# Performance work log

Measured on AMD Instinct MI355X. Metric: run time of the kernel, lower is better.

Reference implementation:

```python
import jax, jax.numpy as jnp
import numpy as np

NUM_HEADS = 16
HEAD_SIZE = 64
MAX_POS = 2048  # config.max_position_embeddings


def setup_inputs() -> dict:
    key = jax.random.key(0)
    ks = jax.random.split(key, 8)
    B, Lq, Lk, D = 4, 1024, 2048, 1024
    s = 1.0 / np.sqrt(D)
    return {
        "hidden_states": jax.random.normal(ks[0], (B, Lk, D), jnp.float32),
        "query_hidden_states": jax.random.normal(ks[1], (B, Lq, D), jnp.float32),
        "attention_mask": jnp.zeros((B, 1, 1, Lk), jnp.float32),
        "Wq": jax.random.normal(ks[2], (D, D), jnp.float32) * s,
        "bq": jnp.zeros((D,), jnp.float32),
        "Wk": jax.random.normal(ks[3], (D, D), jnp.float32) * s,
        "bk": jnp.zeros((D,), jnp.float32),
        "Wv": jax.random.normal(ks[4], (D, D), jnp.float32) * s,
        "bv": jnp.zeros((D,), jnp.float32),
        "dist_emb": jax.random.normal(ks[5], (2 * MAX_POS - 1, HEAD_SIZE), jnp.float32) * 0.02,
    }


def _split_heads(x):
    # [B, L, H*Dh] -> [B, H, L, Dh]
    B, L, _ = x.shape
    return x.reshape(B, L, NUM_HEADS, HEAD_SIZE).transpose(0, 2, 1, 3)


def reference(hidden_states, query_hidden_states, attention_mask, Wq, bq, Wk, bk, Wv, bv, dist_emb):
    # Linear projections (torch Linear: x @ W.T + b)
    q = _split_heads(query_hidden_states @ Wq.T + bq)   # [B,H,Lq,Dh]
    k = _split_heads(hidden_states @ Wk.T + bk)          # [B,H,Lk,Dh]
    v = _split_heads(hidden_states @ Wv.T + bv)          # [B,H,Lk,Dh]

    scores = jnp.einsum('bhld,bhrd->bhlr', q, k)         # [B,H,Lq,Lk]

    # relative_key_query positional scores
    Lq, Lk = q.shape[2], k.shape[2]
    distance = jnp.arange(Lq)[:, None] - jnp.arange(Lk)[None, :]
    pe = dist_emb[distance + MAX_POS - 1]                # [Lq,Lk,Dh]
    scores = scores + jnp.einsum('bhld,lrd->bhlr', q, pe) + jnp.einsum('bhrd,lrd->bhlr', k, pe)

    scores = scores / np.sqrt(HEAD_SIZE) + attention_mask
    probs = jax.nn.softmax(scores, axis=-1)              # dropout p=0 (eval)
    ctx = jnp.einsum('bhlr,bhrd->bhld', probs, v)        # [B,H,Lq,Dh]
    B = ctx.shape[0]
    return ctx.transpose(0, 2, 1, 3).reshape(B, Lq, NUM_HEADS * HEAD_SIZE)
```

## Files before the change

### kernel.cpp

```cpp
#include <hip/hip_runtime.h>
#include <hip/hip_bf16.h>

#define B_   4
#define H_   16
#define LQ   1024
#define LK   2048
#define D_   1024
#define DH   64

typedef __attribute__((ext_vector_type(8))) short  short8;
typedef __attribute__((ext_vector_type(4))) float  float4_;
typedef __attribute__((ext_vector_type(4))) unsigned int uint4_;

static __device__ __forceinline__ float bf2f(unsigned short u) {
    unsigned int x = ((unsigned int)u) << 16;
    return __builtin_bit_cast(float, x);
}
static __device__ __forceinline__ unsigned short f2bf(float f) {
    unsigned int x = __builtin_bit_cast(unsigned int, f);
    unsigned int lsb = (x >> 16) & 1u;
    x += 0x7fffu + lsb;
    return (unsigned short)(x >> 16);
}
static __device__ __forceinline__ unsigned int pack2(float a, float b) {
    __hip_bfloat162 h = __float22bfloat162_rn(make_float2(a, b));
    unsigned int r;
    __builtin_memcpy(&r, &h, 4);
    return r;
}

#define MFMA(a, b, c) __builtin_amdgcn_mfma_f32_16x16x32_bf16((a), (b), (c), 0, 0, 0)

#define G2ROW(tl) ((tl) * 144 + ((tl) >> 2) * 8)

__global__ __launch_bounds__(256) void conv_kernel(
    const float* __restrict__ Wq, const float* __restrict__ Wk,
    const float* __restrict__ Wv, const float* __restrict__ Eg,
    unsigned short* __restrict__ cWq, unsigned short* __restrict__ cWk,
    unsigned short* __restrict__ cWv, unsigned short* __restrict__ cEb)
{
    int bid = blockIdx.x;
    const float* src; unsigned short* dst; int nch;
    if (bid < 512)       { src = Wq; dst = cWq;              nch = 131072; }
    else if (bid < 1024) { src = Wk; dst = cWk; bid -= 512;  nch = 131072; }
    else if (bid < 1536) { src = Wv; dst = cWv; bid -= 1024; nch = 131072; }
    else                 { src = Eg; dst = cEb; bid -= 1536; nch = 32760;  }
    int ch = bid * 256 + threadIdx.x;
    if (ch >= nch) return;
    const float* s = src + (size_t)ch * 8;
    float4_ v0 = *(const float4_*)s, v1 = *(const float4_*)(s + 4);
    uint4_ o;
    o[0] = pack2(v0[0], v0[1]); o[1] = pack2(v0[2], v0[3]);
    o[2] = pack2(v1[0], v1[1]); o[3] = pack2(v1[2], v1[3]);
    *(uint4_*)(dst + (size_t)ch * 8) = o;
}

__global__ __launch_bounds__(256) void proj_kernel(
    const float* __restrict__ Xq, const float* __restrict__ Xk,
    const unsigned short* __restrict__ Wq, const float* __restrict__ bq,
    const unsigned short* __restrict__ Wk, const float* __restrict__ bk,
    const unsigned short* __restrict__ Wv, const float* __restrict__ bv,
    unsigned short* __restrict__ Qh, unsigned short* __restrict__ Kh,
    unsigned short* __restrict__ VT)
{
    __shared__ short smem[17408];
    short* As = smem;
    short* Bs = smem + 5120;
    short* Cs = smem;

    int bid = blockIdx.x;
    int which, tm, tn;
    const float *X, *bias; const unsigned short* W;
    if (bid < 256)      { which = 0; int t = bid;       tm = t >> 3; tn = t & 7; X = Xq; W = Wq; bias = bq; }
    else if (bid < 768) { which = 1; int t = bid - 256; tm = t >> 3; tn = t & 7; X = Xk; W = Wk; bias = bk; }
    else                { which = 2; int t = bid - 768; tm = t >> 3; tn = t & 7; X = Xk; W = Wv; bias = bv; }

    int tid  = threadIdx.x;
    int wave = tid >> 6, lane = tid & 63;
    int wr = (wave >> 1) * 64, wc = (wave & 1) * 64;
    int m0 = tm * 128, n0 = tn * 128;

    float4_ acc[4][4];
    for (int a = 0; a < 4; ++a) for (int c = 0; c < 4; ++c) acc[a][c] = (float4_)0.0f;

    int srow = tid >> 2, skp = (tid & 3) * 8;
    const float*          Ag = X + (size_t)(m0 + srow) * D_ + skp;
    const unsigned short* Bg = W + (size_t)(n0 + srow) * D_ + skp;
    int lrow = lane & 15, lk8 = (lane >> 4) * 8;

    for (int kt = 0; kt < 32; ++kt) {
        int k0 = kt * 32;
        for (int i = 0; i < 2; ++i) {
            int row = srow + i * 64;
            const float* pa = Ag + (size_t)i * 64 * D_ + k0;
            float4_ a0 = *(const float4_*)(pa);
            float4_ a1 = *(const float4_*)(pa + 4);
            uint4_ va;
            va[0] = pack2(a0[0], a0[1]); va[1] = pack2(a0[2], a0[3]);
            va[2] = pack2(a1[0], a1[1]); va[3] = pack2(a1[2], a1[3]);
            uint4_ vb = *(const uint4_*)(Bg + (size_t)i * 64 * D_ + k0);
            *(uint4_*)(&As[row * 40 + skp]) = va;
            *(uint4_*)(&Bs[row * 40 + skp]) = vb;
        }
        __syncthreads();
        short8 af[4], bfr[4];
        for (int rt = 0; rt < 4; ++rt) af[rt]  = *(const short8*)(&As[(wr + rt * 16 + lrow) * 40 + lk8]);
        for (int ct = 0; ct < 4; ++ct) bfr[ct] = *(const short8*)(&Bs[(wc + ct * 16 + lrow) * 40 + lk8]);
        for (int rt = 0; rt < 4; ++rt)
            for (int ct = 0; ct < 4; ++ct)
                acc[rt][ct] = MFMA(af[rt], bfr[ct], acc[rt][ct]);
        __syncthreads();
    }

    int lrow4 = (lane >> 4) * 4, lcol = lane & 15;
    if (which < 2) {
        int lsh = (which == 0) ? 10 : 11;
        int Lm1 = (1 << lsh) - 1;
        unsigned short* dst = (which == 0) ? Qh : Kh;
        for (int rt = 0; rt < 4; ++rt)
            for (int ct = 0; ct < 4; ++ct)
                for (int i = 0; i < 4; ++i) {
                    int m = m0 + wr + rt * 16 + lrow4 + i;
                    int n = n0 + wc + ct * 16 + lcol;
                    float v = acc[rt][ct][i] + bias[n];
                    int b = m >> lsh, s = m & Lm1;
                    int h = n >> 6, d = n & 63;
                    dst[((size_t)((b * H_ + h) << lsh) + (size_t)s) * DH + d] = f2bf(v);
                }
    } else {
        for (int rt = 0; rt < 4; ++rt)
            for (int ct = 0; ct < 4; ++ct)
                for (int i = 0; i < 4; ++i) {
                    int rl = wr + rt * 16 + lrow4 + i;
                    int cl = wc + ct * 16 + lcol;
                    float v = acc[rt][ct][i] + bias[n0 + cl];
                    Cs[cl * 136 + rl] = (short)f2bf(v);
                }
        __syncthreads();
        int b = m0 >> 11, r0 = m0 & 2047;
        int c = tid >> 1, half = tid & 1;
        int n = n0 + c, h = n >> 6, d = n & 63;
        unsigned short* dstp = VT + ((size_t)(b * H_ + h) * DH + d) * LK + r0 + half * 64;
        for (int j = 0; j < 8; ++j) {
            uint4_ v = *(const uint4_*)(&Cs[c * 136 + half * 64 + j * 8]);
            *(uint4_*)(dstp + j * 8) = v;
        }
    }
}

__global__ __launch_bounds__(256, 2) void attn_kernel(
    const unsigned short* __restrict__ Qh, const unsigned short* __restrict__ Kh,
    const unsigned short* __restrict__ VT, const unsigned short* __restrict__ Eb,
    const float* __restrict__ mask, float* __restrict__ out)
{
    __shared__ short smem[27776];
    short* Qs  = smem;
    short* Ks  = smem;
    short* VTs = smem + 4608;
    short* Es  = smem + 9216;
    short* G2  = smem + 18432;
    short* Ps  = G2;

    int bid = blockIdx.x;
    int l0 = (bid & 15) * 64;
    int bh = bid >> 4;
    int b  = bh >> 4, h = bh & 15;
    int tid = threadIdx.x, wave = tid >> 6, lane = tid & 63;
    int lr = lane & 15, lk8 = (lane >> 4) * 8, lr4 = (lane >> 4) * 4;

    for (int i = 0; i < 2; ++i) {
        int idx = tid + 256 * i, row = idx >> 3, g = (idx & 7) * 8;
        *(uint4_*)(&Qs[row * 72 + g]) =
            *(const uint4_*)(Qh + ((size_t)(bh * LQ + l0 + row)) * DH + g);
    }
    __syncthreads();
    short8 aq0 = *(const short8*)(&Qs[(wave * 16 + lr) * 72 + lk8]);
    short8 aq1 = *(const short8*)(&Qs[(wave * 16 + lr) * 72 + 32 + lk8]);

    float m_i[4], l_i[4];
    float4_ Oacc[4];
    for (int i = 0; i < 4; ++i) { m_i[i] = -1e30f; l_i[i] = 0.f; Oacc[i] = (float4_)0.f; }

    const unsigned short* Kbase = Kh + (size_t)bh * LK * DH;
    const unsigned short* Vbase = VT + (size_t)bh * DH * LK;

    int srow = tid >> 3;
    int sg   = (tid & 7) * 8;

    uint4_ kr0, kr1, vr0, vr1, er0, er1, er2, er3;
    auto load_tiles = [&](int it2) {
        int r0_ = it2 * 64, jb_ = l0 - r0_ + 1984;
        kr0 = *(const uint4_*)(Kbase + (size_t)(r0_ + srow) * DH + sg);
        kr1 = *(const uint4_*)(Kbase + (size_t)(r0_ + srow + 32) * DH + sg);
        vr0 = *(const uint4_*)(Vbase + (size_t)srow * LK + r0_ + sg);
        vr1 = *(const uint4_*)(Vbase + (size_t)(srow + 32) * LK + r0_ + sg);
        er0 = *(const uint4_*)(Eb + (size_t)(jb_ + srow) * DH + sg);
        er1 = *(const uint4_*)(Eb + (size_t)(jb_ + srow + 32) * DH + sg);
        er2 = *(const uint4_*)(Eb + (size_t)(jb_ + srow + 64) * DH + sg);
        er3 = *(const uint4_*)(Eb + (size_t)(jb_ + srow + 96) * DH + sg);
    };
    load_tiles(0);

    for (int it = 0; it < 32; ++it) {
        int r0 = it * 64;

        __syncthreads();
        *(uint4_*)(&Ks[srow * 72 + sg])         = kr0;
        *(uint4_*)(&Ks[(srow + 32) * 72 + sg])  = kr1;
        *(uint4_*)(&VTs[srow * 72 + sg])        = vr0;
        *(uint4_*)(&VTs[(srow + 32) * 72 + sg]) = vr1;
        *(uint4_*)(&Es[srow * 72 + sg])         = er0;
        *(uint4_*)(&Es[(srow + 32) * 72 + sg])  = er1;
        *(uint4_*)(&Es[(srow + 64) * 72 + sg])  = er2;
        *(uint4_*)(&Es[(srow + 96) * 72 + sg])  = er3;
        __syncthreads();
        if (it < 31) load_tiles(it + 1);

        float4_ Sacc[4];
        for (int c = 0; c < 4; ++c) {
            short8 b0 = *(const short8*)(&Ks[(c * 16 + lr) * 72 + lk8]);
            short8 b1 = *(const short8*)(&Ks[(c * 16 + lr) * 72 + 32 + lk8]);
            float4_ s = (float4_)0.f;
            s = MFMA(aq0, b0, s);
            s = MFMA(aq1, b1, s);
            Sacc[c] = s;
        }

        short8 ak0 = *(const short8*)(&Ks[(wave * 16 + lr) * 72 + lk8]);
        short8 ak1 = *(const short8*)(&Ks[(wave * 16 + lr) * 72 + 32 + lk8]);
        unsigned int gqp[5][2], gkp[5][2];
        for (int tt = 0; tt < 5; ++tt) {
            int tqi = wave + tt;
            short8 e0 = *(const short8*)(&Es[(tqi * 16 + lr) * 72 + lk8]);
            short8 e1 = *(const short8*)(&Es[(tqi * 16 + lr) * 72 + 32 + lk8]);
            float4_ g = (float4_)0.f;
            g = MFMA(aq0, e0, g); g = MFMA(aq1, e1, g);
            gqp[tt][0] = pack2(g[0], g[1]); gqp[tt][1] = pack2(g[2], g[3]);
            int tk = (3 - wave) + tt;
            short8 f0 = *(const short8*)(&Es[(tk * 16 + lr) * 72 + lk8]);
            short8 f1 = *(const short8*)(&Es[(tk * 16 + lr) * 72 + 32 + lk8]);
            float4_ gg = (float4_)0.f;
            gg = MFMA(ak0, f0, gg); gg = MFMA(ak1, f1, gg);
            gkp[tt][0] = pack2(gg[0], gg[1]); gkp[tt][1] = pack2(gg[2], gg[3]);
        }

        for (int tt = 0; tt < 5; ++tt) {
            int uq = (wave + tt) * 16 + lr;
            int uk = (3 - wave + tt) * 16 + lr;
            for (int i = 0; i < 4; ++i) {
                int row = wave * 16 + lr4 + i;
                unsigned int wq32 = gqp[tt][i >> 1], wk32 = gkp[tt][i >> 1];
                unsigned short vq = (unsigned short)((i & 1) ? (wq32 >> 16) : (wq32 & 0xffff));
                unsigned short vk = (unsigned short)((i & 1) ? (wk32 >> 16) : (wk32 & 0xffff));
                int tr = row - uq + 63;
                if ((unsigned)tr < 64u)
                    G2[G2ROW(row) + ((tr & 15) << 3) + (((tr >> 4)) << 1)] = (short)vq;
                int tl = uk + row - 63;
                if ((unsigned)tl < 64u)
                    G2[G2ROW(tl) + ((row & 15) << 3) + (((row >> 4)) << 1) + 1] = (short)vk;
            }
        }
        __syncthreads();

        float mk[4];
        for (int c = 0; c < 4; ++c) mk[c] = mask[b * LK + r0 + c * 16 + lr];
        for (int i = 0; i < 4; ++i) {
            int tl = wave * 16 + lr4 + i;
            short8 gv = *(const short8*)(&G2[G2ROW(tl) + (lr << 3)]);
            float scv[4], mx = -1e30f;
            for (int c = 0; c < 4; ++c) {
                float sq = bf2f((unsigned short)gv[2 * c]);
                float sk = bf2f((unsigned short)gv[2 * c + 1]);
                float sc = (Sacc[c][i] + sq + sk) * 0.125f + mk[c];
                scv[c] = sc;
                mx = fmaxf(mx, sc);
            }
            for (int off = 1; off < 16; off <<= 1) mx = fmaxf(mx, __shfl_xor(mx, off, 64));
            float mnew = fmaxf(m_i[i], mx);
            float alpha = __expf(m_i[i] - mnew);
            m_i[i] = mnew;
            float e0 = __expf(scv[0] - mnew), e1 = __expf(scv[1] - mnew);
            float e2 = __expf(scv[2] - mnew), e3 = __expf(scv[3] - mnew);
            unsigned int p01 = pack2(e0, e1), p23 = pack2(e2, e3);
            float rs = bf2f((unsigned short)(p01 & 0xffff)) + bf2f((unsigned short)(p01 >> 16))
                     + bf2f((unsigned short)(p23 & 0xffff)) + bf2f((unsigned short)(p23 >> 16));
            for (int off = 1; off < 16; off <<= 1) rs += __shfl_xor(rs, off, 64);
            l_i[i] = l_i[i] * alpha + rs;
            for (int nt = 0; nt < 4; ++nt) Oacc[nt][i] *= alpha;
            Ps[G2ROW(tl) +  0 + lr] = (short)(unsigned short)(p01 & 0xffff);
            Ps[G2ROW(tl) + 16 + lr] = (short)(unsigned short)(p01 >> 16);
            Ps[G2ROW(tl) + 32 + lr] = (short)(unsigned short)(p23 & 0xffff);
            Ps[G2ROW(tl) + 48 + lr] = (short)(unsigned short)(p23 >> 16);
        }
        short8 ap0 = *(const short8*)(&Ps[G2ROW(wave * 16 + lr) + lk8]);
        short8 ap1 = *(const short8*)(&Ps[G2ROW(wave * 16 + lr) + 32 + lk8]);
        for (int nt = 0; nt < 4; ++nt) {
            short8 v0 = *(const short8*)(&VTs[(nt * 16 + lr) * 72 + lk8]);
            short8 v1 = *(const short8*)(&VTs[(nt * 16 + lr) * 72 + 32 + lk8]);
            Oacc[nt] = MFMA(ap0, v0, Oacc[nt]);
            Oacc[nt] = MFMA(ap1, v1, Oacc[nt]);
        }
    }

    for (int nt = 0; nt < 4; ++nt)
        for (int i = 0; i < 4; ++i) {
            int row = l0 + wave * 16 + lr4 + i;
            int col = h * 64 + nt * 16 + lr;
            out[(size_t)(b * LQ + row) * D_ + col] = Oacc[nt][i] / l_i[i];
        }
}

extern "C" void kernel_launch(void* const* d_in, const int* in_sizes, int n_in,
                              void* d_out, int out_size, void* d_ws, size_t ws_size,
                              hipStream_t stream) {
    (void)in_sizes; (void)n_in; (void)out_size; (void)ws_size;
    const float* Xk   = (const float*)d_in[0];
    const float* Xq   = (const float*)d_in[1];
    const float* mask = (const float*)d_in[2];
    const float* Wq   = (const float*)d_in[3];
    const float* bq   = (const float*)d_in[4];
    const float* Wk   = (const float*)d_in[5];
    const float* bk   = (const float*)d_in[6];
    const float* Wv   = (const float*)d_in[7];
    const float* bv   = (const float*)d_in[8];
    const float* Eg   = (const float*)d_in[9];

    unsigned short* Qh  = (unsigned short*)d_ws;
    unsigned short* Kh  = Qh  + (size_t)4194304;
    unsigned short* VT  = Kh  + (size_t)8388608;
    unsigned short* cWq = VT  + (size_t)8388608;
    unsigned short* cWk = cWq + (size_t)1048576;
    unsigned short* cWv = cWk + (size_t)1048576;
    unsigned short* cEb = cWv + (size_t)1048576;
    float* o = (float*)d_out;

    conv_kernel<<<1664, 256, 0, stream>>>(Wq, Wk, Wv, Eg, cWq, cWk, cWv, cEb);
    proj_kernel<<<1280, 256, 0, stream>>>(Xq, Xk, cWq, bq, cWk, bk, cWv, bv, Qh, Kh, VT);
    attn_kernel<<<1024, 256, 0, stream>>>(Qh, Kh, VT, cEb, mask, o);
}
```

Measured before the change: 487.3 us.

## Prefetch projection GEMM tiles and reuse the relative-embedding window as a ring buffer

The projection GEMM now loads the next k-tile into registers while the current tile's MFMAs run, using one barrier per iteration instead of two. The attention kernel keeps the 128-row distance-embedding window in shared memory as a ring buffer indexed by a phase offset. Since the window slides by 64 rows per step, only the 64 new rows are fetched each iteration instead of all 128. The q/k positional MFMAs are merged into one loop that reads each embedding fragment once and feeds both products. This cuts global traffic and LDS reads, at the cost of more live registers and more complex indexing.

```diff
diff --git a/kernel.cpp b/kernel.cpp
--- a/kernel.cpp
+++ b/kernel.cpp
@@ -88,29 +88,40 @@
     const unsigned short* Bg = W + (size_t)(n0 + srow) * D_ + skp;
     int lrow = lane & 15, lk8 = (lane >> 4) * 8;
 
+    float4_ pa0[2], pa1[2]; uint4_ pb[2];
+    auto load_kt = [&](int kt) {
+        int k0 = kt * 32;
+        #pragma unroll
+        for (int i = 0; i < 2; ++i) {
+            const float* pa = Ag + (size_t)i * 64 * D_ + k0;
+            pa0[i] = *(const float4_*)(pa);
+            pa1[i] = *(const float4_*)(pa + 4);
+            pb[i]  = *(const uint4_*)(Bg + (size_t)i * 64 * D_ + k0);
+        }
+    };
+    load_kt(0);
+
     for (int kt = 0; kt < 32; ++kt) {
-        int k0 = kt * 32;
+        __syncthreads();
+        #pragma unroll
         for (int i = 0; i < 2; ++i) {
             int row = srow + i * 64;
-            const float* pa = Ag + (size_t)i * 64 * D_ + k0;
-            float4_ a0 = *(const float4_*)(pa);
-            float4_ a1 = *(const float4_*)(pa + 4);
             uint4_ va;
-            va[0] = pack2(a0[0], a0[1]); va[1] = pack2(a0[2], a0[3]);
-            va[2] = pack2(a1[0], a1[1]); va[3] = pack2(a1[2], a1[3]);
-            uint4_ vb = *(const uint4_*)(Bg + (size_t)i * 64 * D_ + k0);
+            va[0] = pack2(pa0[i][0], pa0[i][1]); va[1] = pack2(pa0[i][2], pa0[i][3]);
+            va[2] = pack2(pa1[i][0], pa1[i][1]); va[3] = pack2(pa1[i][2], pa1[i][3]);
             *(uint4_*)(&As[row * 40 + skp]) = va;
-            *(uint4_*)(&Bs[row * 40 + skp]) = vb;
-        }
-        __syncthreads();
+            *(uint4_*)(&Bs[row * 40 + skp]) = pb[i];
+        }
+        __syncthreads();
+        if (kt < 31) load_kt(kt + 1);
         short8 af[4], bfr[4];
         for (int rt = 0; rt < 4; ++rt) af[rt]  = *(const short8*)(&As[(wr + rt * 16 + lrow) * 40 + lk8]);
         for (int ct = 0; ct < 4; ++ct) bfr[ct] = *(const short8*)(&Bs[(wc + ct * 16 + lrow) * 40 + lk8]);
         for (int rt = 0; rt < 4; ++rt)
             for (int ct = 0; ct < 4; ++ct)
                 acc[rt][ct] = MFMA(af[rt], bfr[ct], acc[rt][ct]);
-        __syncthreads();
-    }
+    }
+    __syncthreads();
 
     int lrow4 = (lane >> 4) * 4, lcol = lane & 15;
     if (which < 2) {
@@ -196,27 +207,35 @@
         vr1 = *(const uint4_*)(Vbase + (size_t)(srow + 32) * LK + r0_ + sg);
         er0 = *(const uint4_*)(Eb + (size_t)(jb_ + srow) * DH + sg);
         er1 = *(const uint4_*)(Eb + (size_t)(jb_ + srow + 32) * DH + sg);
-        er2 = *(const uint4_*)(Eb + (size_t)(jb_ + srow + 64) * DH + sg);
-        er3 = *(const uint4_*)(Eb + (size_t)(jb_ + srow + 96) * DH + sg);
     };
     load_tiles(0);
+    {
+        int jb0 = l0 + 1984;
+        er2 = *(const uint4_*)(Eb + (size_t)(jb0 + srow + 64) * DH + sg);
+        er3 = *(const uint4_*)(Eb + (size_t)(jb0 + srow + 96) * DH + sg);
+    }
 
     for (int it = 0; it < 32; ++it) {
         int r0 = it * 64;
+        int ph = (l0 + 1984 - r0) & 127;
 
         __syncthreads();
         *(uint4_*)(&Ks[srow * 72 + sg])         = kr0;
         *(uint4_*)(&Ks[(srow + 32) * 72 + sg])  = kr1;
         *(uint4_*)(&VTs[srow * 72 + sg])        = vr0;
         *(uint4_*)(&VTs[(srow + 32) * 72 + sg]) = vr1;
-        *(uint4_*)(&Es[srow * 72 + sg])         = er0;
-        *(uint4_*)(&Es[(srow + 32) * 72 + sg])  = er1;
-        *(uint4_*)(&Es[(srow + 64) * 72 + sg])  = er2;
-        *(uint4_*)(&Es[(srow + 96) * 72 + sg])  = er3;
+        *(uint4_*)(&Es[((ph + srow) & 127) * 72 + sg])      = er0;
+        *(uint4_*)(&Es[((ph + srow + 32) & 127) * 72 + sg]) = er1;
+        if (it == 0) {
+            *(uint4_*)(&Es[((ph + srow + 64) & 127) * 72 + sg]) = er2;
+            *(uint4_*)(&Es[((ph + srow + 96) & 127) * 72 + sg]) = er3;
+        }
         __syncthreads();
         if (it < 31) load_tiles(it + 1);
 
+        short8 ak0, ak1;
         float4_ Sacc[4];
+        #pragma unroll
         for (int c = 0; c < 4; ++c) {
             short8 b0 = *(const short8*)(&Ks[(c * 16 + lr) * 72 + lk8]);
             short8 b1 = *(const short8*)(&Ks[(c * 16 + lr) * 72 + 32 + lk8]);
@@ -224,40 +243,47 @@
             s = MFMA(aq0, b0, s);
             s = MFMA(aq1, b1, s);
             Sacc[c] = s;
-        }
-
-        short8 ak0 = *(const short8*)(&Ks[(wave * 16 + lr) * 72 + lk8]);
-        short8 ak1 = *(const short8*)(&Ks[(wave * 16 + lr) * 72 + 32 + lk8]);
-        unsigned int gqp[5][2], gkp[5][2];
-        for (int tt = 0; tt < 5; ++tt) {
-            int tqi = wave + tt;
-            short8 e0 = *(const short8*)(&Es[(tqi * 16 + lr) * 72 + lk8]);
-            short8 e1 = *(const short8*)(&Es[(tqi * 16 + lr) * 72 + 32 + lk8]);
-            float4_ g = (float4_)0.f;
-            g = MFMA(aq0, e0, g); g = MFMA(aq1, e1, g);
-            gqp[tt][0] = pack2(g[0], g[1]); gqp[tt][1] = pack2(g[2], g[3]);
-            int tk = (3 - wave) + tt;
-            short8 f0 = *(const short8*)(&Es[(tk * 16 + lr) * 72 + lk8]);
-            short8 f1 = *(const short8*)(&Es[(tk * 16 + lr) * 72 + 32 + lk8]);
-            float4_ gg = (float4_)0.f;
-            gg = MFMA(ak0, f0, gg); gg = MFMA(ak1, f1, gg);
-            gkp[tt][0] = pack2(gg[0], gg[1]); gkp[tt][1] = pack2(gg[2], gg[3]);
-        }
-
-        for (int tt = 0; tt < 5; ++tt) {
-            int uq = (wave + tt) * 16 + lr;
-            int uk = (3 - wave + tt) * 16 + lr;
-            for (int i = 0; i < 4; ++i) {
-                int row = wave * 16 + lr4 + i;
-                unsigned int wq32 = gqp[tt][i >> 1], wk32 = gkp[tt][i >> 1];
-                unsigned short vq = (unsigned short)((i & 1) ? (wq32 >> 16) : (wq32 & 0xffff));
-                unsigned short vk = (unsigned short)((i & 1) ? (wk32 >> 16) : (wk32 & 0xffff));
-                int tr = row - uq + 63;
-                if ((unsigned)tr < 64u)
-                    G2[G2ROW(row) + ((tr & 15) << 3) + (((tr >> 4)) << 1)] = (short)vq;
-                int tl = uk + row - 63;
-                if ((unsigned)tl < 64u)
-                    G2[G2ROW(tl) + ((row & 15) << 3) + (((row >> 4)) << 1) + 1] = (short)vk;
+            if (c == 0 || c == wave) { ak0 = b0; ak1 = b1; }
+        }
+
+        #pragma unroll
+        for (int t = 0; t < 8; ++t) {
+            int dq = t - wave;
+            int dk = t - 3 + wave;
+            bool needq = (unsigned)dq < 5u;
+            bool needk = (unsigned)dk < 5u;
+            if (!(needq || needk)) continue;
+            int es = ((ph + t * 16 + lr) & 127) * 72;
+            short8 e0 = *(const short8*)(&Es[es + lk8]);
+            short8 e1 = *(const short8*)(&Es[es + 32 + lk8]);
+            int u = t * 16 + lr;
+            if (needq) {
+                float4_ g = (float4_)0.f;
+                g = MFMA(aq0, e0, g); g = MFMA(aq1, e1, g);
+                unsigned int p0 = pack2(g[0], g[1]), p1 = pack2(g[2], g[3]);
+                #pragma unroll
+                for (int i = 0; i < 4; ++i) {
+                    int row = wave * 16 + lr4 + i;
+                    unsigned int w32 = (i >> 1) ? p1 : p0;
+                    unsigned short vq = (unsigned short)((i & 1) ? (w32 >> 16) : (w32 & 0xffff));
+                    int tr = row - u + 63;
+                    if ((unsigned)tr < 64u)
+                        G2[G2ROW(row) + ((tr & 15) << 3) + ((tr >> 4) << 1)] = (short)vq;
+                }
+            }
+            if (needk) {
+                float4_ gg = (float4_)0.f;
+                gg = MFMA(ak0, e0, gg); gg = MFMA(ak1, e1, gg);
+                unsigned int q0 = pack2(gg[0], gg[1]), q1 = pack2(gg[2], gg[3]);
+                #pragma unroll
+                for (int i = 0; i < 4; ++i) {
+                    int row = wave * 16 + lr4 + i;
+                    unsigned int w32 = (i >> 1) ? q1 : q0;
+                    unsigned short vk = (unsigned short)((i & 1) ? (w32 >> 16) : (w32 & 0xffff));
+                    int tl = u + row - 63;
+                    if ((unsigned)tl < 64u)
+                        G2[G2ROW(tl) + ((row & 15) << 3) + ((row >> 4) << 1) + 1] = (short)vk;
+                }
             }
         }
         __syncthreads();
```

Measured after the change: 487.3 us. No clear change (+0.0%).

## Pre-convert activations to bf16 and load GEMM tiles directly into LDS

Applied to the files above, without the earlier changes.

The conversion kernel now also converts the query and key hidden states to bf16, staging the key copy in the output buffer, so the projection GEMM no longer reads fp32 activations repeatedly and packs them per tile. The projection kernel uses global_load_lds 16-byte direct loads into an XOR-swizzled 64-wide k-tile, halving the k-loop trip count. This removes redundant fp32 traffic and VGPR round trips, at the cost of an extra conversion pass over the activations and reuse of the output buffer as scratch.

```diff
diff --git a/kernel.cpp b/kernel.cpp
--- a/kernel.cpp
+++ b/kernel.cpp
@@ -33,18 +33,26 @@
 
 #define G2ROW(tl) ((tl) * 144 + ((tl) >> 2) * 8)
 
+#define GLOAD_LDS16(g, l) __builtin_amdgcn_global_load_lds( \
+    (const __attribute__((address_space(1))) unsigned int*)(const void*)(g), \
+    (__attribute__((address_space(3))) unsigned int*)(void*)(l), 16, 0, 0)
+
 __global__ __launch_bounds__(256) void conv_kernel(
     const float* __restrict__ Wq, const float* __restrict__ Wk,
     const float* __restrict__ Wv, const float* __restrict__ Eg,
+    const float* __restrict__ Xq, const float* __restrict__ Xk,
     unsigned short* __restrict__ cWq, unsigned short* __restrict__ cWk,
-    unsigned short* __restrict__ cWv, unsigned short* __restrict__ cEb)
+    unsigned short* __restrict__ cWv, unsigned short* __restrict__ cEb,
+    unsigned short* __restrict__ cXq, unsigned short* __restrict__ cXk)
 {
     int bid = blockIdx.x;
     const float* src; unsigned short* dst; int nch;
-    if (bid < 512)       { src = Wq; dst = cWq;              nch = 131072; }
-    else if (bid < 1024) { src = Wk; dst = cWk; bid -= 512;  nch = 131072; }
-    else if (bid < 1536) { src = Wv; dst = cWv; bid -= 1024; nch = 131072; }
-    else                 { src = Eg; dst = cEb; bid -= 1536; nch = 32760;  }
+    if (bid < 512)       { src = Wq; dst = cWq;              nch = 131072;  }
+    else if (bid < 1024) { src = Wk; dst = cWk; bid -= 512;  nch = 131072;  }
+    else if (bid < 1536) { src = Wv; dst = cWv; bid -= 1024; nch = 131072;  }
+    else if (bid < 1664) { src = Eg; dst = cEb; bid -= 1536; nch = 32760;   }
+    else if (bid < 3712) { src = Xq; dst = cXq; bid -= 1664; nch = 524288;  }
+    else                 { src = Xk; dst = cXk; bid -= 3712; nch = 1048576; }
     int ch = bid * 256 + threadIdx.x;
     if (ch >= nch) return;
     const float* s = src + (size_t)ch * 8;
@@ -56,7 +64,7 @@
 }
 
 __global__ __launch_bounds__(256) void proj_kernel(
-    const float* __restrict__ Xq, const float* __restrict__ Xk,
+    const unsigned short* __restrict__ Xq, const unsigned short* __restrict__ Xk,
     const unsigned short* __restrict__ Wq, const float* __restrict__ bq,
     const unsigned short* __restrict__ Wk, const float* __restrict__ bk,
     const unsigned short* __restrict__ Wv, const float* __restrict__ bv,
@@ -65,12 +73,12 @@
 {
     __shared__ short smem[17408];
     short* As = smem;
-    short* Bs = smem + 5120;
+    short* Bs = smem + 8192;
     short* Cs = smem;
 
     int bid = blockIdx.x;
     int which, tm, tn;
-    const float *X, *bias; const unsigned short* W;
+    const unsigned short *X; const float* bias; const unsigned short* W;
     if (bid < 256)      { which = 0; int t = bid;       tm = t >> 3; tn = t & 7; X = Xq; W = Wq; bias = bq; }
     else if (bid < 768) { which = 1; int t = bid - 256; tm = t >> 3; tn = t & 7; X = Xk; W = Wk; bias = bk; }
     else                { which = 2; int t = bid - 768; tm = t >> 3; tn = t & 7; X = Xk; W = Wv; bias = bv; }
@@ -83,32 +91,39 @@
     float4_ acc[4][4];
     for (int a = 0; a < 4; ++a) for (int c = 0; c < 4; ++c) acc[a][c] = (float4_)0.0f;
 
-    int srow = tid >> 2, skp = (tid & 3) * 8;
-    const float*          Ag = X + (size_t)(m0 + srow) * D_ + skp;
-    const unsigned short* Bg = W + (size_t)(n0 + srow) * D_ + skp;
+    int rl = lane >> 3;
+    int chs = (lane & 7) ^ rl;
+    const unsigned short* Asrc = X + (size_t)(m0 + wave * 32 + rl) * D_ + (chs << 3);
+    const unsigned short* Bsrc = W + (size_t)(n0 + wave * 32 + rl) * D_ + (chs << 3);
+
     int lrow = lane & 15, lk8 = (lane >> 4) * 8;
-
-    for (int kt = 0; kt < 32; ++kt) {
-        int k0 = kt * 32;
-        for (int i = 0; i < 2; ++i) {
-            int row = srow + i * 64;
-            const float* pa = Ag + (size_t)i * 64 * D_ + k0;
-            float4_ a0 = *(const float4_*)(pa);
-            float4_ a1 = *(const float4_*)(pa + 4);
-            uint4_ va;
-            va[0] = pack2(a0[0], a0[1]); va[1] = pack2(a0[2], a0[3]);
-            va[2] = pack2(a1[0], a1[1]); va[3] = pack2(a1[2], a1[3]);
-            uint4_ vb = *(const uint4_*)(Bg + (size_t)i * 64 * D_ + k0);
-            *(uint4_*)(&As[row * 40 + skp]) = va;
-            *(uint4_*)(&Bs[row * 40 + skp]) = vb;
-        }
-        __syncthreads();
-        short8 af[4], bfr[4];
-        for (int rt = 0; rt < 4; ++rt) af[rt]  = *(const short8*)(&As[(wr + rt * 16 + lrow) * 40 + lk8]);
-        for (int ct = 0; ct < 4; ++ct) bfr[ct] = *(const short8*)(&Bs[(wc + ct * 16 + lrow) * 40 + lk8]);
-        for (int rt = 0; rt < 4; ++rt)
+    int swz = lane & 7;
+
+    for (int kt = 0; kt < 16; ++kt) {
+        int k0 = kt * 64;
+        #pragma unroll
+        for (int c = 0; c < 4; ++c) {
+            GLOAD_LDS16(Asrc + (size_t)(c * 8) * D_ + k0, &As[(wave * 32 + c * 8) * 64]);
+            GLOAD_LDS16(Bsrc + (size_t)(c * 8) * D_ + k0, &Bs[(wave * 32 + c * 8) * 64]);
+        }
+        __syncthreads();
+        #pragma unroll
+        for (int kk = 0; kk < 64; kk += 32) {
+            int cgrp = (kk + lk8) >> 3;
+            int coff = ((cgrp ^ swz) << 3);
+            short8 af[4], bfr[4];
+            #pragma unroll
+            for (int rt = 0; rt < 4; ++rt)
+                af[rt]  = *(const short8*)(&As[(wr + rt * 16 + lrow) * 64 + coff]);
+            #pragma unroll
             for (int ct = 0; ct < 4; ++ct)
-                acc[rt][ct] = MFMA(af[rt], bfr[ct], acc[rt][ct]);
+                bfr[ct] = *(const short8*)(&Bs[(wc + ct * 16 + lrow) * 64 + coff]);
+            #pragma unroll
+            for (int rt = 0; rt < 4; ++rt)
+                #pragma unroll
+                for (int ct = 0; ct < 4; ++ct)
+                    acc[rt][ct] = MFMA(af[rt], bfr[ct], acc[rt][ct]);
+        }
         __syncthreads();
     }
 
@@ -131,10 +146,10 @@
         for (int rt = 0; rt < 4; ++rt)
             for (int ct = 0; ct < 4; ++ct)
                 for (int i = 0; i < 4; ++i) {
-                    int rl = wr + rt * 16 + lrow4 + i;
-                    int cl = wc + ct * 16 + lcol;
+                    int rl2 = wr + rt * 16 + lrow4 + i;
+                    int cl  = wc + ct * 16 + lcol;
                     float v = acc[rt][ct][i] + bias[n0 + cl];
-                    Cs[cl * 136 + rl] = (short)f2bf(v);
+                    Cs[cl * 136 + rl2] = (short)f2bf(v);
                 }
         __syncthreads();
         int b = m0 >> 11, r0 = m0 & 2047;
@@ -332,9 +347,12 @@
     unsigned short* cWk = cWq + (size_t)1048576;
     unsigned short* cWv = cWk + (size_t)1048576;
     unsigned short* cEb = cWv + (size_t)1048576;
+    unsigned short* cXq = cEb + (size_t)262144;
+    unsigned short* cXk = (unsigned short*)d_out;
     float* o = (float*)d_out;
 
-    conv_kernel<<<1664, 256, 0, stream>>>(Wq, Wk, Wv, Eg, cWq, cWk, cWv, cEb);
-    proj_kernel<<<1280, 256, 0, stream>>>(Xq, Xk, cWq, bq, cWk, bk, cWv, bv, Qh, Kh, VT);
+    conv_kernel<<<7808, 256, 0, stream>>>(Wq, Wk, Wv, Eg, Xq, Xk,
+                                          cWq, cWk, cWv, cEb, cXq, cXk);
+    proj_kernel<<<1280, 256, 0, stream>>>(cXq, cXk, cWq, bq, cWk, bk, cWv, bv, Qh, Kh, VT);
     attn_kernel<<<1024, 256, 0, stream>>>(Qh, Kh, VT, cEb, mask, o);
 }
```

After: 446.1 us. 1.09x faster.
